# Kernel optimization log

Measured on AMD Instinct MI355X. Metric: run time of the kernel, lower is better.

## Reference

```python
import jax, jax.numpy as jnp
import numpy as np

K_ACTIVE = 32
MULTI_K = 64
AUX_K = 64
DEAD_THRESH = 256


def setup_inputs() -> dict:
    key = jax.random.key(0)
    ks = jax.random.split(key, 4)
    B, D, M = 4096, 1024, 16384
    x = jax.random.normal(ks[0], (B, D), dtype=jnp.float32)
    enc_w = jax.random.normal(ks[1], (M, D), dtype=jnp.float32) / np.sqrt(D)
    dec_w = jax.random.normal(ks[2], (D, M), dtype=jnp.float32) / np.sqrt(M)
    input_bias = jnp.zeros((D,), dtype=jnp.float32)
    neuron_bias = jnp.zeros((M,), dtype=jnp.float32)
    steps = jax.random.randint(ks[3], (M,), 0, 512).astype(jnp.int64)
    return {"x": x, "enc_w": enc_w, "dec_w": dec_w,
            "input_bias": input_bias, "neuron_bias": neuron_bias, "steps": steps}


def reference(x, enc_w, dec_w, input_bias, neuron_bias, steps):
    # encode: center, linear (no bias), add neuron bias, relu
    x_cent = x - input_bias                                   # [B, D]
    pre_act = x_cent @ enc_w.T + neuron_bias                  # [B, M]
    acts = jax.nn.relu(pre_act)
    B, M = acts.shape

    # training path: global batch-wide top-(K*B) across flattened activations
    flat = acts.reshape(-1)                                   # [B*M]
    topk_vals, topk_idx = jax.lax.top_k(flat, K_ACTIVE * B)
    activ = jnp.zeros_like(flat).at[topk_idx].set(topk_vals).reshape(B, M)

    # multi-k branch: per-row top-k on pre-activations, relu, scatter, decode
    mvals, midx = jax.lax.top_k(pre_act, MULTI_K)             # [B, MULTI_K]
    mvals = jax.nn.relu(mvals)
    rows = jnp.arange(B)[:, None]
    multik_activ = jnp.zeros_like(pre_act).at[rows, midx].set(mvals)
    multik_recon = multik_activ @ dec_w.T + input_bias        # [B, D]

    # main reconstruction
    recon = activ @ dec_w.T + input_bias                      # [B, D]

    # dead-neuron bookkeeping + aux top-k over dead neurons
    steps = steps + 1
    active = activ.sum(axis=0) > 0                            # [M]
    steps = jnp.where(active, jnp.zeros_like(steps), steps)
    dead_mask = (steps > DEAD_THRESH).astype(pre_act.dtype)   # [M]
    dead_pre = pre_act * dead_mask                            # [B, M]
    aux_vals, aux_idx = jax.lax.top_k(dead_pre, AUX_K)        # [B, AUX_K]
    aux_vals = jax.nn.relu(aux_vals)

    return recon, activ, multik_recon, aux_vals, aux_idx
```

## Files before the change

### kernel.cpp

```cpp
#include <hip/hip_runtime.h>

#define K_ACTIVE 32
#define MULTI_K 64
#define AUX_K 64
#define DEAD_THRESH 256
#define BUF_CAP 262144u
#define SORT_CAP 4096

typedef unsigned int u32;
typedef unsigned long long u64;
typedef unsigned short ushort_t;
typedef __bf16 bf16x8 __attribute__((ext_vector_type(8)));
typedef float f32x4 __attribute__((ext_vector_type(4)));

__device__ __forceinline__ u32 fmap_signed_bits(u32 u) {
  return (u & 0x80000000u) ? ~u : (u | 0x80000000u);
}

__device__ __forceinline__ u32 bf16_rne(float f) {
  u32 u = __float_as_uint(f);
  return (u + 0x7FFFu + ((u >> 16) & 1u)) >> 16;
}

__device__ __forceinline__ void gload16(const void* g, void* s) {
  __builtin_amdgcn_global_load_lds(
      (const __attribute__((address_space(1))) void*)g,
      (__attribute__((address_space(3))) void*)s, 16, 0, 0);
}

__global__ void transpose_k(const float* __restrict__ in, float* __restrict__ out, int D, int M) {
  __shared__ float tile[32][33];
  const int bx = blockIdx.x * 32;
  const int by = blockIdx.y * 32;
  const int tx = threadIdx.x, ty = threadIdx.y;
  #pragma unroll
  for (int i = 0; i < 32; i += 8)
    tile[ty + i][tx] = in[(size_t)(by + ty + i) * M + bx + tx];
  __syncthreads();
  #pragma unroll
  for (int i = 0; i < 32; i += 8)
    out[(size_t)(bx + ty + i) * D + by + tx] = tile[tx][ty + i];
}

__global__ void convA_k(const float* __restrict__ X, const float* __restrict__ IB,
                        ushort_t* __restrict__ AH, ushort_t* __restrict__ AL, int D) {
  const int idx = blockIdx.x * 256 + threadIdx.x;
  const int row = idx >> 7;
  const int dpos = (idx & 127) << 3;
  const float4* xr = reinterpret_cast<const float4*>(X + (size_t)row * D + dpos);
  const float4* br = reinterpret_cast<const float4*>(IB + dpos);
  float4 x0 = xr[0], x1 = xr[1], b0 = br[0], b1 = br[1];
  float c[8] = {x0.x - b0.x, x0.y - b0.y, x0.z - b0.z, x0.w - b0.w,
                x1.x - b1.x, x1.y - b1.y, x1.z - b1.z, x1.w - b1.w};
  u32 hw[4], lw[4];
  #pragma unroll
  for (int j = 0; j < 4; ++j) {
    u32 h0 = bf16_rne(c[2 * j]), h1 = bf16_rne(c[2 * j + 1]);
    float r0 = c[2 * j] - __uint_as_float(h0 << 16);
    float r1 = c[2 * j + 1] - __uint_as_float(h1 << 16);
    hw[j] = h0 | (h1 << 16);
    lw[j] = bf16_rne(r0) | (bf16_rne(r1) << 16);
  }
  reinterpret_cast<uint4*>(AH)[idx] = make_uint4(hw[0], hw[1], hw[2], hw[3]);
  reinterpret_cast<uint4*>(AL)[idx] = make_uint4(lw[0], lw[1], lw[2], lw[3]);
}

__global__ void convW_k(const float* __restrict__ W,
                        ushort_t* __restrict__ WH, ushort_t* __restrict__ WL) {
  const int idx = blockIdx.x * 256 + threadIdx.x;
  const float4* wr = reinterpret_cast<const float4*>(W) + (size_t)idx * 2;
  float4 x0 = wr[0], x1 = wr[1];
  float c[8] = {x0.x, x0.y, x0.z, x0.w, x1.x, x1.y, x1.z, x1.w};
  u32 hw[4], lw[4];
  #pragma unroll
  for (int j = 0; j < 4; ++j) {
    u32 h0 = bf16_rne(c[2 * j]), h1 = bf16_rne(c[2 * j + 1]);
    float r0 = c[2 * j] - __uint_as_float(h0 << 16);
    float r1 = c[2 * j + 1] - __uint_as_float(h1 << 16);
    hw[j] = h0 | (h1 << 16);
    lw[j] = bf16_rne(r0) | (bf16_rne(r1) << 16);
  }
  reinterpret_cast<uint4*>(WH)[idx] = make_uint4(hw[0], hw[1], hw[2], hw[3]);
  reinterpret_cast<uint4*>(WL)[idx] = make_uint4(lw[0], lw[1], lw[2], lw[3]);
}

__global__ __launch_bounds__(256) void gemm_mfma(
    const ushort_t* __restrict__ AH, const ushort_t* __restrict__ AL,
    const ushort_t* __restrict__ WH, const ushort_t* __restrict__ WL,
    const float* __restrict__ NB, float* __restrict__ OUT, int M) {
  __shared__ ushort_t sA[128 * 64];
  __shared__ ushort_t sB[128 * 64];
  const int tid = threadIdx.x;
  const int wave = tid >> 6, lane = tid & 63;
  const int bm = blockIdx.y * 128, bn = blockIdx.x * 128;
  const int wm = wave & 1, wn = wave >> 1;

  f32x4 acc[4][4];
  #pragma unroll
  for (int i = 0; i < 4; ++i)
    #pragma unroll
    for (int j = 0; j < 4; ++j) acc[i][j] = (f32x4){0.f, 0.f, 0.f, 0.f};

  int rowA[4], cbA[4];
  #pragma unroll
  for (int r = 0; r < 4; ++r) {
    int o = ((wave << 2) + r) * 1024 + lane * 16;
    rowA[r] = o >> 7;
    cbA[r] = o & 127;
  }
  const int cl = lane & 15, kg = lane >> 4;

  for (int kt = 0; kt < 48; ++kt) {
    const int ph = kt >> 4;
    const size_t kb = (size_t)((kt & 15) << 6) * 2;
    const ushort_t* Asrc = (ph == 1) ? AL : AH;
    const ushort_t* Bsrc = (ph == 2) ? WL : WH;
    #pragma unroll
    for (int r = 0; r < 4; ++r) {
      gload16((const char*)Asrc + ((size_t)(bm + rowA[r]) * 2048 + kb + cbA[r]),
              (char*)sA + (((wave << 2) + r) << 10));
      gload16((const char*)Bsrc + ((size_t)(bn + rowA[r]) * 2048 + kb + cbA[r]),
              (char*)sB + (((wave << 2) + r) << 10));
    }
    __syncthreads();
    #pragma unroll
    for (int ks = 0; ks < 2; ++ks) {
      const int kk = ks * 32 + kg * 8;
      bf16x8 af[4], bfr[4];
      #pragma unroll
      for (int mi = 0; mi < 4; ++mi)
        af[mi] = *reinterpret_cast<const bf16x8*>(&sA[(wm * 64 + mi * 16 + cl) * 64 + kk]);
      #pragma unroll
      for (int ni = 0; ni < 4; ++ni)
        bfr[ni] = *reinterpret_cast<const bf16x8*>(&sB[(wn * 64 + ni * 16 + cl) * 64 + kk]);
      #pragma unroll
      for (int mi = 0; mi < 4; ++mi)
        #pragma unroll
        for (int ni = 0; ni < 4; ++ni)
          acc[mi][ni] = __builtin_amdgcn_mfma_f32_16x16x32_bf16(af[mi], bfr[ni], acc[mi][ni], 0, 0, 0);
    }
    __syncthreads();
  }

  const int rg = lane >> 4;
  #pragma unroll
  for (int ni = 0; ni < 4; ++ni) {
    const int col = bn + wn * 64 + ni * 16 + cl;
    const float nbv = NB[col];
    #pragma unroll
    for (int mi = 0; mi < 4; ++mi) {
      const int row0 = bm + wm * 64 + mi * 16 + rg * 4;
      #pragma unroll
      for (int r = 0; r < 4; ++r)
        OUT[(size_t)(row0 + r) * M + col] = acc[mi][ni][r] + nbv;
    }
  }
}

__global__ void hist1_k(const float* __restrict__ P, size_t N, u32* __restrict__ GH) {
  __shared__ u32 h[2048];
  const int tid = threadIdx.x;
  for (int i = tid; i < 2048; i += 256) h[i] = 0;
  __syncthreads();
  u32 l0 = 0;
  const size_t step = (size_t)gridDim.x * 256;
  for (size_t i = (size_t)blockIdx.x * 256 + tid; i < N; i += step) {
    float v = P[i];
    float a = (v > 0.f) ? v : 0.f;
    u32 b = __float_as_uint(a) >> 21;
    if (b) atomicAdd(&h[b], 1u); else ++l0;
  }
  if (l0) atomicAdd(&h[0], l0);
  __syncthreads();
  for (int i = tid; i < 2048; i += 256) if (h[i]) atomicAdd(&GH[i], h[i]);
}

__global__ void scan_k(const u32* __restrict__ H, u32* __restrict__ PRM, u32 K, int phase) {
  __shared__ u32 suf[256];
  const int t = threadIdx.x;
  u32 h[8], ls[8];
  #pragma unroll
  for (int j = 0; j < 8; ++j) h[j] = H[t * 8 + j];
  u32 run = 0;
  #pragma unroll
  for (int j = 7; j >= 0; --j) { run += h[j]; ls[j] = run; }
  suf[t] = run;
  __syncthreads();
  for (int off = 1; off < 256; off <<= 1) {
    u32 v = (t + off < 256) ? suf[t + off] : 0u;
    __syncthreads();
    suf[t] += v;
    __syncthreads();
  }
  const u32 rightOf = (t < 255) ? suf[t + 1] : 0u;
  const u32 base = (phase == 2) ? PRM[1] : 0u;
  #pragma unroll
  for (int j = 0; j < 8; ++j) {
    u32 Sb = base + rightOf + ls[j];
    u32 Sb1 = base + rightOf + ((j < 7) ? ls[j + 1] : 0u);
    if (Sb >= K && Sb1 < K) {
      int b = t * 8 + j;
      if (phase == 1) { PRM[0] = (u32)b; PRM[1] = Sb1; }
      else { PRM[2] = (PRM[0] << 11) | (u32)b; PRM[3] = K - Sb1; }
    }
  }
}

__global__ void hist2_k(const float* __restrict__ P, size_t N, const u32* __restrict__ PRM, u32* __restrict__ GH) {
  const u32 b1 = PRM[0];
  const size_t step = (size_t)gridDim.x * blockDim.x;
  for (size_t i = (size_t)blockIdx.x * blockDim.x + threadIdx.x; i < N; i += step) {
    float v = P[i];
    float a = (v > 0.f) ? v : 0.f;
    u32 u = __float_as_uint(a);
    if ((u >> 21) == b1) atomicAdd(&GH[(u >> 10) & 2047u], 1u);
  }
}

__global__ void collect_k(const float* __restrict__ P, size_t N, u32* __restrict__ PRM,
                          float* __restrict__ BV, u32* __restrict__ BI) {
  const u32 pc = PRM[2];
  const size_t step = (size_t)gridDim.x * blockDim.x;
  for (size_t i = (size_t)blockIdx.x * blockDim.x + threadIdx.x; i < N; i += step) {
    float v = P[i];
    float a = (v > 0.f) ? v : 0.f;
    u32 u = __float_as_uint(a);
    if ((u >> 10) == pc) {
      u32 pos = atomicAdd(&PRM[8], 1u);
      if (pos < BUF_CAP) { BV[pos] = a; BI[pos] = (u32)i; }
    }
  }
}

__global__ void sortmark_k(u32* __restrict__ PRM, const float* __restrict__ BV, const u32* __restrict__ BI,
                           float* __restrict__ SV, u32* __restrict__ SI, u32* __restrict__ CF, int M) {
  __shared__ u64 keys[SORT_CAP];
  const int tid = threadIdx.x;
  u32 nb = PRM[8]; if (nb > SORT_CAP) nb = SORT_CAP;
  const u32 krem = PRM[3];
  if (nb == 0) { if (tid == 0) PRM[5] = 0; return; }
  u32 np = 1; while (np < nb) np <<= 1;
  for (u32 i = tid; i < np; i += 256)
    keys[i] = (i < nb) ? ((((u64)__float_as_uint(BV[i])) << 32) | (u64)(0xFFFFFFFFu - BI[i])) : 0ull;
  __syncthreads();
  for (u32 k = 2; k <= np; k <<= 1) {
    for (u32 j = k >> 1; j > 0; j >>= 1) {
      for (u32 i = tid; i < np; i += 256) {
        u32 ixj = i ^ j;
        if (ixj > i) {
          u64 a = keys[i], b = keys[ixj];
          bool up = ((i & k) == 0);
          if (up ? (a < b) : (a > b)) { keys[i] = b; keys[ixj] = a; }
        }
      }
      __syncthreads();
    }
  }
  u32 nsel = krem < nb ? krem : nb;
  for (u32 t = tid; t < nsel; t += 256) {
    u64 kk = keys[t];
    u32 flat = 0xFFFFFFFFu - (u32)(kk & 0xFFFFFFFFull);
    float val = __uint_as_float((u32)(kk >> 32));
    SI[t] = flat; SV[t] = val;
    if (val > 0.f) CF[flat % (u32)M] = 1u;
  }
  if (tid == 0) PRM[5] = nsel;
}

struct TopkShared {
  u32 hist[256];
  u32 eqcnt[256];
  u32 prefix, need, scnt;
  int selN[64];
  float selV[64];
};

template<bool ZSKIP>
__device__ void row_topk64(const float (&v)[64], int tid, TopkShared* S) {
  const int lane = tid & 63;
  u32 zp = 0, zn = 0;
  if (ZSKIP) {
    #pragma unroll
    for (int j = 0; j < 64; ++j) {
      u32 ub = __float_as_uint(v[j]);
      if (ub == 0u) ++zp;
      else if (ub == 0x80000000u) ++zn;
    }
    for (int o = 32; o > 0; o >>= 1) { zp += __shfl_down(zp, o); zn += __shfl_down(zn, o); }
  }
  if (tid == 0) S->scnt = 0;
  u32 pref = 0, need = 64;
  for (int p = 0; p < 4; ++p) {
    const int sh = 24 - 8 * p;
    S->hist[tid] = 0;
    __syncthreads();
    #pragma unroll
    for (int j = 0; j < 64; ++j) {
      u32 ub = __float_as_uint(v[j]);
      if (ZSKIP && ((ub << 1) == 0u)) continue;
      u32 mu = fmap_signed_bits(ub);
      if (p == 0 || (mu >> (sh + 8)) == pref)
        atomicAdd(&S->hist[(mu >> sh) & 255u], 1u);
    }
    if (ZSKIP && lane == 0) {
      const u32 mup = 0x80000000u, mun = 0x7FFFFFFFu;
      if (zp && (p == 0 || (mup >> (sh + 8)) == pref)) atomicAdd(&S->hist[(mup >> sh) & 255u], zp);
      if (zn && (p == 0 || (mun >> (sh + 8)) == pref)) atomicAdd(&S->hist[(mun >> sh) & 255u], zn);
    }
    __syncthreads();
    for (int off = 1; off < 256; off <<= 1) {
      u32 t2 = (tid + off < 256) ? S->hist[tid + off] : 0u;
      __syncthreads();
      S->hist[tid] += t2;
      __syncthreads();
    }
    u32 Sb = S->hist[tid];
    u32 Sb1 = (tid < 255) ? S->hist[tid + 1] : 0u;
    if (Sb >= need && Sb1 < need) {
      S->prefix = (pref << 8) | (u32)tid;
      S->need = need - Sb1;
    }
    __syncthreads();
    pref = S->prefix; need = S->need;
  }
  const u32 muc = pref, neq = need;
  u32 myeq = 0;
  #pragma unroll
  for (int j = 0; j < 64; ++j) {
    u32 mu = fmap_signed_bits(__float_as_uint(v[j]));
    if (mu > muc) {
      u32 pos = atomicAdd(&S->scnt, 1u);
      S->selN[pos] = tid * 64 + j;
      S->selV[pos] = v[j];
    } else if (mu == muc) ++myeq;
  }
  S->eqcnt[tid] = myeq;
  __syncthreads();
  for (int off = 1; off < 256; off <<= 1) {
    u32 t2 = (tid >= off) ? S->eqcnt[tid - off] : 0u;
    __syncthreads();
    S->eqcnt[tid] += t2;
    __syncthreads();
  }
  const u32 a0 = S->scnt;
  u32 g = S->eqcnt[tid] - myeq;
  #pragma unroll
  for (int j = 0; j < 64; ++j) {
    u32 mu = fmap_signed_bits(__float_as_uint(v[j]));
    if (mu == muc) {
      if (g < neq) { S->selN[a0 + g] = tid * 64 + j; S->selV[a0 + g] = v[j]; }
      ++g;
    }
  }
  __syncthreads();
}

__launch_bounds__(256)
__global__ void rowk_multik(const float* __restrict__ PRE, const float* __restrict__ WT,
                            const float* __restrict__ IB, float* __restrict__ MR,
                            u32* __restrict__ CF, const u32* __restrict__ PRM, int M, int D) {
  __shared__ TopkShared S;
  const int b = blockIdx.x, tid = threadIdx.x;
  const float* rowp = PRE + (size_t)b * M + tid * 64;
  float v[64];
  #pragma unroll
  for (int j = 0; j < 16; ++j) {
    float4 t = reinterpret_cast<const float4*>(rowp)[j];
    v[4 * j + 0] = t.x; v[4 * j + 1] = t.y; v[4 * j + 2] = t.z; v[4 * j + 3] = t.w;
  }
  const u32 pc = PRM[2];
  #pragma unroll
  for (int j = 0; j < 64; ++j) {
    float a = (v[j] > 0.f) ? v[j] : 0.f;
    if (((__float_as_uint(a) >> 10) > pc) && (a > 0.f)) atomicOr(&CF[tid * 64 + j], 1u);
  }
  row_topk64<false>(v, tid, &S);
  const int d0 = tid * 4;
  float4 acc = *reinterpret_cast<const float4*>(IB + d0);
  for (int i = 0; i < 64; ++i) {
    float w = S.selV[i] > 0.f ? S.selV[i] : 0.f;
    if (w > 0.f) {
      const float4 wv = *reinterpret_cast<const float4*>(WT + (size_t)S.selN[i] * D + d0);
      acc.x = fmaf(w, wv.x, acc.x); acc.y = fmaf(w, wv.y, acc.y);
      acc.z = fmaf(w, wv.z, acc.z); acc.w = fmaf(w, wv.w, acc.w);
    }
  }
  *reinterpret_cast<float4*>(MR + (size_t)b * D + d0) = acc;
}

__global__ void dead_k(const u32* __restrict__ CF, const int* __restrict__ ST,
                       u32* __restrict__ DW, int M) {
  int w = blockIdx.x * blockDim.x + threadIdx.x;
  if (w >= M / 32) return;
  u32 bits = 0;
  for (int i = 0; i < 32; ++i) {
    int n = w * 32 + i;
    if (CF[n] == 0 && (ST[n] + 1) > DEAD_THRESH) bits |= (1u << i);
  }
  DW[w] = bits;
}

__launch_bounds__(256)
__global__ void rowk_aux(const float* __restrict__ PRE, const u32* __restrict__ DW,
                         float* __restrict__ AV, float* __restrict__ AI, int M) {
  __shared__ TopkShared S;
  __shared__ u64 skey[64];
  __shared__ int sN[64];
  __shared__ float sV[64];
  const int b = blockIdx.x, tid = threadIdx.x;
  const float* rowp = PRE + (size_t)b * M + tid * 64;
  float v[64];
  #pragma unroll
  for (int j = 0; j < 16; ++j) {
    float4 t = reinterpret_cast<const float4*>(rowp)[j];
    v[4 * j + 0] = t.x; v[4 * j + 1] = t.y; v[4 * j + 2] = t.z; v[4 * j + 3] = t.w;
  }
  const u32 mw0 = DW[tid * 2], mw1 = DW[tid * 2 + 1];
  #pragma unroll
  for (int j = 0; j < 64; ++j) {
    u32 bit = ((j < 32 ? mw0 : mw1) >> (j & 31)) & 1u;
    v[j] = bit ? v[j] : (v[j] * 0.0f);
  }
  row_topk64<true>(v, tid, &S);
  if (tid < 64) {
    float vv = S.selV[tid];
    int col = S.selN[tid];
    u32 mu = fmap_signed_bits(__float_as_uint(vv));
    skey[tid] = (((u64)mu) << 32) | (u64)(0xFFFFFFFFu - (u32)col);
  }
  __syncthreads();
  if (tid < 64) {
    u64 mine = skey[tid];
    int rank = 0;
    for (int j = 0; j < 64; ++j) rank += (skey[j] > mine) ? 1 : 0;
    sN[rank] = S.selN[tid]; sV[rank] = S.selV[tid];
  }
  __syncthreads();
  if (tid < 64) {
    AV[(size_t)b * AUX_K + tid] = sV[tid] > 0.f ? sV[tid] : 0.f;
    AI[(size_t)b * AUX_K + tid] = (float)sN[tid];
  }
}

__launch_bounds__(256)
__global__ void rowk_scatter(float* __restrict__ ACT, const float* __restrict__ WT,
                             const float* __restrict__ IB, float* __restrict__ RC,
                             const u32* __restrict__ PRM, const float* __restrict__ SV,
                             const u32* __restrict__ SI, int M, int D) {
  __shared__ int ovN[256]; __shared__ float ovV[256]; __shared__ u32 ovc;
  __shared__ int lsN[2048]; __shared__ float lsV[2048]; __shared__ u32 lc;
  const int b = blockIdx.x, tid = threadIdx.x;
  float* rowp = ACT + (size_t)b * M + tid * 64;
  float v[64];
  #pragma unroll
  for (int j = 0; j < 16; ++j) {
    float4 t = reinterpret_cast<const float4*>(rowp)[j];
    v[4 * j + 0] = t.x; v[4 * j + 1] = t.y; v[4 * j + 2] = t.z; v[4 * j + 3] = t.w;
  }
  const u32 pc = PRM[2];
  #pragma unroll
  for (int j = 0; j < 64; ++j) {
    float a = (v[j] > 0.f) ? v[j] : 0.f;
    v[j] = ((__float_as_uint(a) >> 10) > pc) ? a : 0.f;
  }
  if (tid == 0) ovc = 0;
  __syncthreads();
  const u32 nbs = PRM[5];
  for (u32 t = tid; t < nbs; t += 256) {
    u32 flat = SI[t];
    if (flat / (u32)M == (u32)b) {
      u32 p = atomicAdd(&ovc, 1u);
      if (p < 256) { ovN[p] = (int)(flat % (u32)M); ovV[p] = SV[t]; }
    }
  }
  __syncthreads();
  const u32 no = ovc < 256u ? ovc : 256u;
  #pragma unroll
  for (int j = 0; j < 64; ++j) {
    const int col = tid * 64 + j;
    for (u32 i = 0; i < no; ++i) if (ovN[i] == col) v[j] = ovV[i];
  }
  #pragma unroll
  for (int j = 0; j < 16; ++j) {
    float4 t = make_float4(v[4 * j + 0], v[4 * j + 1], v[4 * j + 2], v[4 * j + 3]);
    reinterpret_cast<float4*>(rowp)[j] = t;
  }
  const int d0 = tid * 4;
  float4 acc = *reinterpret_cast<const float4*>(IB + d0);
  for (int cpart = 0; cpart < 8; ++cpart) {
    if (tid == 0) lc = 0;
    __syncthreads();
    if ((tid >> 5) == cpart) {
      #pragma unroll
      for (int j = 0; j < 64; ++j) {
        if (v[j] > 0.f) {
          u32 p = atomicAdd(&lc, 1u);
          lsN[p] = tid * 64 + j; lsV[p] = v[j];
        }
      }
    }
    __syncthreads();
    const u32 n = lc;
    for (u32 i = 0; i < n; ++i) {
      const float w = lsV[i];
      const float4 wv = *reinterpret_cast<const float4*>(WT + (size_t)lsN[i] * D + d0);
      acc.x = fmaf(w, wv.x, acc.x); acc.y = fmaf(w, wv.y, acc.y);
      acc.z = fmaf(w, wv.z, acc.z); acc.w = fmaf(w, wv.w, acc.w);
    }
    __syncthreads();
  }
  *reinterpret_cast<float4*>(RC + (size_t)b * D + d0) = acc;
}

extern "C" void kernel_launch(void* const* d_in, const int* in_sizes, int n_in,
                              void* d_out, int out_size, void* d_ws, size_t ws_size,
                              hipStream_t stream) {
  const float* x  = (const float*)d_in[0];
  const float* ew = (const float*)d_in[1];
  const float* dw = (const float*)d_in[2];
  const float* ib = (const float*)d_in[3];
  const float* nb = (const float*)d_in[4];
  const int* steps = (const int*)d_in[5];
  const int D = in_sizes[3];
  const int M = in_sizes[4];
  const int B = in_sizes[0] / D;
  const u32 K = (u32)(K_ACTIVE * B);

  float* out = (float*)d_out;
  float* recon  = out;
  float* activ  = out + (size_t)B * D;
  float* mrecon = activ + (size_t)B * M;
  float* avals  = mrecon + (size_t)B * D;
  float* aidx   = avals + (size_t)B * AUX_K;

  ushort_t* AH = (ushort_t*)recon;
  ushort_t* AL = (ushort_t*)mrecon;

  char* wsp = (char*)d_ws;
  size_t o = 0;
  auto alloc = [&](size_t bytes) { char* p = wsp + o; o += (bytes + 255) & ~(size_t)255; return p; };
  ushort_t* WH = (ushort_t*)alloc((size_t)M * D * 2);
  ushort_t* WL = (ushort_t*)alloc((size_t)M * D * 2);
  float* WT = (float*)alloc((size_t)M * D * 4);
  u32* H1   = (u32*)alloc(8192);
  u32* H2   = (u32*)alloc(8192);
  u32* PRM  = (u32*)alloc(256);
  u32* CF   = (u32*)alloc((size_t)M * 4);
  u32* DW   = (u32*)alloc((size_t)(M / 32) * 4);
  float* BV = (float*)alloc((size_t)BUF_CAP * 4);
  u32* BI   = (u32*)alloc((size_t)BUF_CAP * 4);
  float* SV = (float*)alloc((size_t)SORT_CAP * 4);
  u32* SI   = (u32*)alloc((size_t)SORT_CAP * 4);
  (void)ws_size; (void)n_in; (void)out_size;

  hipMemsetAsync(H1, 0, 8192, stream);
  hipMemsetAsync(H2, 0, 8192, stream);
  hipMemsetAsync(PRM, 0, 256, stream);
  hipMemsetAsync(CF, 0, (size_t)M * 4, stream);

  convA_k<<<(B * D / 8 + 255) / 256, 256, 0, stream>>>(x, ib, AH, AL, D);
  convW_k<<<((size_t)M * D / 8 + 255) / 256, 256, 0, stream>>>(ew, WH, WL);
  transpose_k<<<dim3(M / 32, D / 32), dim3(32, 8), 0, stream>>>(dw, WT, D, M);
  gemm_mfma<<<dim3(M / 128, B / 128), 256, 0, stream>>>(AH, AL, WH, WL, nb, activ, M);

  const size_t N = (size_t)B * M;
  hist1_k<<<2048, 256, 0, stream>>>(activ, N, H1);
  scan_k<<<1, 256, 0, stream>>>(H1, PRM, K, 1);
  hist2_k<<<2048, 256, 0, stream>>>(activ, N, PRM, H2);
  scan_k<<<1, 256, 0, stream>>>(H2, PRM, K, 2);
  collect_k<<<2048, 256, 0, stream>>>(activ, N, PRM, BV, BI);
  sortmark_k<<<1, 256, 0, stream>>>(PRM, BV, BI, SV, SI, CF, M);
  rowk_multik<<<B, 256, 0, stream>>>(activ, WT, ib, mrecon, CF, PRM, M, D);
  dead_k<<<(M / 32 + 255) / 256, 256, 0, stream>>>(CF, steps, DW, M);
  rowk_aux<<<B, 256, 0, stream>>>(activ, DW, avals, aidx, M);
  rowk_scatter<<<B, 256, 0, stream>>>(activ, WT, ib, recon, PRM, SV, SI, M, D);
}
```

Baseline: 1.824 ms.

## Swizzle GEMM LDS, vectorize histogram passes, fuse per-row top-k kernels into one

Adds an XOR swizzle to the GEMM shared-memory tiles so MFMA fragment reads avoid bank conflicts. Vectorizes the histogram and collect passes to float4 and gives hist1 privatized per-lane shared histograms to cut atomic contention. Moves the active-neuron flag marking into collect_k and fuses the multi-k, aux and scatter row kernels into one kernel, so each pre-activation row is read once instead of three times. The row top-k now uses 16 privatized histograms and wave-shuffle scans in place of shared-memory scans. The costs are larger shared-memory use per block, which may lower occupancy, and more register pressure in the fused kernel.

Result: slower. 2.915 ms (+59.8%).

```diff
diff --git a/kernel.cpp b/kernel.cpp
--- a/kernel.cpp
+++ b/kernel.cpp
@@ -101,12 +101,14 @@
     #pragma unroll
     for (int j = 0; j < 4; ++j) acc[i][j] = (f32x4){0.f, 0.f, 0.f, 0.f};
 
-  int rowA[4], cbA[4];
+  int rowA[4], cbS[4];
   #pragma unroll
   for (int r = 0; r < 4; ++r) {
     int o = ((wave << 2) + r) * 1024 + lane * 16;
-    rowA[r] = o >> 7;
-    cbA[r] = o & 127;
+    int row = o >> 7;
+    int cb = o & 127;
+    rowA[r] = row;
+    cbS[r] = cb ^ ((row & 7) << 4);
   }
   const int cl = lane & 15, kg = lane >> 4;
 
@@ -117,22 +119,28 @@
     const ushort_t* Bsrc = (ph == 2) ? WL : WH;
     #pragma unroll
     for (int r = 0; r < 4; ++r) {
-      gload16((const char*)Asrc + ((size_t)(bm + rowA[r]) * 2048 + kb + cbA[r]),
+      gload16((const char*)Asrc + ((size_t)(bm + rowA[r]) * 2048 + kb + cbS[r]),
               (char*)sA + (((wave << 2) + r) << 10));
-      gload16((const char*)Bsrc + ((size_t)(bn + rowA[r]) * 2048 + kb + cbA[r]),
+      gload16((const char*)Bsrc + ((size_t)(bn + rowA[r]) * 2048 + kb + cbS[r]),
               (char*)sB + (((wave << 2) + r) << 10));
     }
     __syncthreads();
     #pragma unroll
     for (int ks = 0; ks < 2; ++ks) {
-      const int kk = ks * 32 + kg * 8;
+      const int kbyte = ks * 64 + kg * 16;
       bf16x8 af[4], bfr[4];
       #pragma unroll
-      for (int mi = 0; mi < 4; ++mi)
-        af[mi] = *reinterpret_cast<const bf16x8*>(&sA[(wm * 64 + mi * 16 + cl) * 64 + kk]);
+      for (int mi = 0; mi < 4; ++mi) {
+        const int rA = wm * 64 + mi * 16 + cl;
+        af[mi] = *reinterpret_cast<const bf16x8*>(
+            (const char*)sA + rA * 128 + (kbyte ^ ((rA & 7) << 4)));
+      }
       #pragma unroll
-      for (int ni = 0; ni < 4; ++ni)
-        bfr[ni] = *reinterpret_cast<const bf16x8*>(&sB[(wn * 64 + ni * 16 + cl) * 64 + kk]);
+      for (int ni = 0; ni < 4; ++ni) {
+        const int rB = wn * 64 + ni * 16 + cl;
+        bfr[ni] = *reinterpret_cast<const bf16x8*>(
+            (const char*)sB + rB * 128 + (kbyte ^ ((rB & 7) << 4)));
+      }
       #pragma unroll
       for (int mi = 0; mi < 4; ++mi)
         #pragma unroll
@@ -157,22 +165,30 @@
   }
 }
 
-__global__ void hist1_k(const float* __restrict__ P, size_t N, u32* __restrict__ GH) {
-  __shared__ u32 h[2048];
+__global__ void hist1_k(const float4* __restrict__ P4, size_t N4, u32* __restrict__ GH) {
+  __shared__ u32 h[4 * 2049];
   const int tid = threadIdx.x;
-  for (int i = tid; i < 2048; i += 256) h[i] = 0;
-  __syncthreads();
+  for (int i = tid; i < 4 * 2049; i += 256) h[i] = 0;
+  __syncthreads();
+  const int rb = (tid & 3) * 2049;
   u32 l0 = 0;
   const size_t step = (size_t)gridDim.x * 256;
-  for (size_t i = (size_t)blockIdx.x * 256 + tid; i < N; i += step) {
-    float v = P[i];
-    float a = (v > 0.f) ? v : 0.f;
-    u32 b = __float_as_uint(a) >> 21;
-    if (b) atomicAdd(&h[b], 1u); else ++l0;
-  }
-  if (l0) atomicAdd(&h[0], l0);
-  __syncthreads();
-  for (int i = tid; i < 2048; i += 256) if (h[i]) atomicAdd(&GH[i], h[i]);
+  for (size_t i = (size_t)blockIdx.x * 256 + tid; i < N4; i += step) {
+    float4 vv = P4[i];
+    float va[4] = {vv.x, vv.y, vv.z, vv.w};
+    #pragma unroll
+    for (int c = 0; c < 4; ++c) {
+      float a = (va[c] > 0.f) ? va[c] : 0.f;
+      u32 b = __float_as_uint(a) >> 21;
+      if (b) atomicAdd(&h[rb + b], 1u); else ++l0;
+    }
+  }
+  if (l0) atomicAdd(&h[rb], l0);
+  __syncthreads();
+  for (int i = tid; i < 2048; i += 256) {
+    u32 s = h[i] + h[2049 + i] + h[2 * 2049 + i] + h[3 * 2049 + i];
+    if (s) atomicAdd(&GH[i], s);
+  }
 }
 
 __global__ void scan_k(const u32* __restrict__ H, u32* __restrict__ PRM, u32 K, int phase) {
@@ -206,28 +222,40 @@
   }
 }
 
-__global__ void hist2_k(const float* __restrict__ P, size_t N, const u32* __restrict__ PRM, u32* __restrict__ GH) {
+__global__ void hist2_k(const float4* __restrict__ P4, size_t N4, const u32* __restrict__ PRM, u32* __restrict__ GH) {
   const u32 b1 = PRM[0];
   const size_t step = (size_t)gridDim.x * blockDim.x;
-  for (size_t i = (size_t)blockIdx.x * blockDim.x + threadIdx.x; i < N; i += step) {
-    float v = P[i];
-    float a = (v > 0.f) ? v : 0.f;
-    u32 u = __float_as_uint(a);
-    if ((u >> 21) == b1) atomicAdd(&GH[(u >> 10) & 2047u], 1u);
-  }
-}
-
-__global__ void collect_k(const float* __restrict__ P, size_t N, u32* __restrict__ PRM,
-                          float* __restrict__ BV, u32* __restrict__ BI) {
+  for (size_t i = (size_t)blockIdx.x * blockDim.x + threadIdx.x; i < N4; i += step) {
+    float4 vv = P4[i];
+    float va[4] = {vv.x, vv.y, vv.z, vv.w};
+    #pragma unroll
+    for (int c = 0; c < 4; ++c) {
+      float a = (va[c] > 0.f) ? va[c] : 0.f;
+      u32 u = __float_as_uint(a);
+      if ((u >> 21) == b1) atomicAdd(&GH[(u >> 10) & 2047u], 1u);
+    }
+  }
+}
+
+__global__ void collect_k(const float4* __restrict__ P4, size_t N4, u32* __restrict__ PRM,
+                          float* __restrict__ BV, u32* __restrict__ BI,
+                          u32* __restrict__ CF, int M) {
   const u32 pc = PRM[2];
   const size_t step = (size_t)gridDim.x * blockDim.x;
-  for (size_t i = (size_t)blockIdx.x * blockDim.x + threadIdx.x; i < N; i += step) {
-    float v = P[i];
-    float a = (v > 0.f) ? v : 0.f;
-    u32 u = __float_as_uint(a);
-    if ((u >> 10) == pc) {
-      u32 pos = atomicAdd(&PRM[8], 1u);
-      if (pos < BUF_CAP) { BV[pos] = a; BI[pos] = (u32)i; }
+  for (size_t i = (size_t)blockIdx.x * blockDim.x + threadIdx.x; i < N4; i += step) {
+    float4 vv = P4[i];
+    float va[4] = {vv.x, vv.y, vv.z, vv.w};
+    #pragma unroll
+    for (int c = 0; c < 4; ++c) {
+      float a = (va[c] > 0.f) ? va[c] : 0.f;
+      u32 u = __float_as_uint(a);
+      u32 bin = u >> 10;
+      if (bin == pc) {
+        u32 pos = atomicAdd(&PRM[8], 1u);
+        if (pos < BUF_CAP) { BV[pos] = a; BI[pos] = (u32)(i * 4 + c); }
+      } else if (bin > pc) {
+        if (a > 0.f) CF[(u32)((i * 4 + c) % (size_t)M)] = 1u;
+      }
     }
   }
 }
@@ -267,127 +295,6 @@
   if (tid == 0) PRM[5] = nsel;
 }
 
-struct TopkShared {
-  u32 hist[256];
-  u32 eqcnt[256];
-  u32 prefix, need, scnt;
-  int selN[64];
-  float selV[64];
-};
-
-template<bool ZSKIP>
-__device__ void row_topk64(const float (&v)[64], int tid, TopkShared* S) {
-  const int lane = tid & 63;
-  u32 zp = 0, zn = 0;
-  if (ZSKIP) {
-    #pragma unroll
-    for (int j = 0; j < 64; ++j) {
-      u32 ub = __float_as_uint(v[j]);
-      if (ub == 0u) ++zp;
-      else if (ub == 0x80000000u) ++zn;
-    }
-    for (int o = 32; o > 0; o >>= 1) { zp += __shfl_down(zp, o); zn += __shfl_down(zn, o); }
-  }
-  if (tid == 0) S->scnt = 0;
-  u32 pref = 0, need = 64;
-  for (int p = 0; p < 4; ++p) {
-    const int sh = 24 - 8 * p;
-    S->hist[tid] = 0;
-    __syncthreads();
-    #pragma unroll
-    for (int j = 0; j < 64; ++j) {
-      u32 ub = __float_as_uint(v[j]);
-      if (ZSKIP && ((ub << 1) == 0u)) continue;
-      u32 mu = fmap_signed_bits(ub);
-      if (p == 0 || (mu >> (sh + 8)) == pref)
-        atomicAdd(&S->hist[(mu >> sh) & 255u], 1u);
-    }
-    if (ZSKIP && lane == 0) {
-      const u32 mup = 0x80000000u, mun = 0x7FFFFFFFu;
-      if (zp && (p == 0 || (mup >> (sh + 8)) == pref)) atomicAdd(&S->hist[(mup >> sh) & 255u], zp);
-      if (zn && (p == 0 || (mun >> (sh + 8)) == pref)) atomicAdd(&S->hist[(mun >> sh) & 255u], zn);
-    }
-    __syncthreads();
-    for (int off = 1; off < 256; off <<= 1) {
-      u32 t2 = (tid + off < 256) ? S->hist[tid + off] : 0u;
-      __syncthreads();
-      S->hist[tid] += t2;
-      __syncthreads();
-    }
-    u32 Sb = S->hist[tid];
-    u32 Sb1 = (tid < 255) ? S->hist[tid + 1] : 0u;
-    if (Sb >= need && Sb1 < need) {
-      S->prefix = (pref << 8) | (u32)tid;
-      S->need = need - Sb1;
-    }
-    __syncthreads();
-    pref = S->prefix; need = S->need;
-  }
-  const u32 muc = pref, neq = need;
-  u32 myeq = 0;
-  #pragma unroll
-  for (int j = 0; j < 64; ++j) {
-    u32 mu = fmap_signed_bits(__float_as_uint(v[j]));
-    if (mu > muc) {
-      u32 pos = atomicAdd(&S->scnt, 1u);
-      S->selN[pos] = tid * 64 + j;
-      S->selV[pos] = v[j];
-    } else if (mu == muc) ++myeq;
-  }
-  S->eqcnt[tid] = myeq;
-  __syncthreads();
-  for (int off = 1; off < 256; off <<= 1) {
-    u32 t2 = (tid >= off) ? S->eqcnt[tid - off] : 0u;
-    __syncthreads();
-    S->eqcnt[tid] += t2;
-    __syncthreads();
-  }
-  const u32 a0 = S->scnt;
-  u32 g = S->eqcnt[tid] - myeq;
-  #pragma unroll
-  for (int j = 0; j < 64; ++j) {
-    u32 mu = fmap_signed_bits(__float_as_uint(v[j]));
-    if (mu == muc) {
-      if (g < neq) { S->selN[a0 + g] = tid * 64 + j; S->selV[a0 + g] = v[j]; }
-      ++g;
-    }
-  }
-  __syncthreads();
-}
-
-__launch_bounds__(256)
-__global__ void rowk_multik(const float* __restrict__ PRE, const float* __restrict__ WT,
-                            const float* __restrict__ IB, float* __restrict__ MR,
-                            u32* __restrict__ CF, const u32* __restrict__ PRM, int M, int D) {
-  __shared__ TopkShared S;
-  const int b = blockIdx.x, tid = threadIdx.x;
-  const float* rowp = PRE + (size_t)b * M + tid * 64;
-  float v[64];
-  #pragma unroll
-  for (int j = 0; j < 16; ++j) {
-    float4 t = reinterpret_cast<const float4*>(rowp)[j];
-    v[4 * j + 0] = t.x; v[4 * j + 1] = t.y; v[4 * j + 2] = t.z; v[4 * j + 3] = t.w;
-  }
-  const u32 pc = PRM[2];
-  #pragma unroll
-  for (int j = 0; j < 64; ++j) {
-    float a = (v[j] > 0.f) ? v[j] : 0.f;
-    if (((__float_as_uint(a) >> 10) > pc) && (a > 0.f)) atomicOr(&CF[tid * 64 + j], 1u);
-  }
-  row_topk64<false>(v, tid, &S);
-  const int d0 = tid * 4;
-  float4 acc = *reinterpret_cast<const float4*>(IB + d0);
-  for (int i = 0; i < 64; ++i) {
-    float w = S.selV[i] > 0.f ? S.selV[i] : 0.f;
-    if (w > 0.f) {
-      const float4 wv = *reinterpret_cast<const float4*>(WT + (size_t)S.selN[i] * D + d0);
-      acc.x = fmaf(w, wv.x, acc.x); acc.y = fmaf(w, wv.y, acc.y);
-      acc.z = fmaf(w, wv.z, acc.z); acc.w = fmaf(w, wv.w, acc.w);
-    }
-  }
-  *reinterpret_cast<float4*>(MR + (size_t)b * D + d0) = acc;
-}
-
 __global__ void dead_k(const u32* __restrict__ CF, const int* __restrict__ ST,
                        u32* __restrict__ DW, int M) {
   int w = blockIdx.x * blockDim.x + threadIdx.x;
@@ -400,28 +307,158 @@
   DW[w] = bits;
 }
 
+struct TopkSh {
+  union {
+    u32 hist[16 * 257];
+    struct { int N[2048]; float V[2048]; } ls;
+  } u;
+  u32 wred[4];
+  u32 prefix, need, scnt;
+  int selN[64];
+  float selV[64];
+};
+
+#define VALX(j) (MASKED ? ((((((j) < 32) ? mw0 : mw1) >> ((j) & 31)) & 1u) ? v[(j)] : v[(j)] * 0.0f) : v[(j)])
+
+template<bool MASKED>
+__device__ void row_topk64(const float (&v)[64], u32 mw0, u32 mw1, int tid, TopkSh* S) {
+  const int lane = tid & 63, wid = tid >> 6;
+  u32 zp = 0, zn = 0;
+  if (MASKED) {
+    #pragma unroll
+    for (int j = 0; j < 64; ++j) {
+      u32 ub = __float_as_uint(VALX(j));
+      zp += (ub == 0u);
+      zn += (ub == 0x80000000u);
+    }
+    #pragma unroll
+    for (int o = 32; o > 0; o >>= 1) { zp += __shfl_down(zp, o); zn += __shfl_down(zn, o); }
+  }
+  u32 pref = 0, need = 64;
+  for (int p = 0; p < 4; ++p) {
+    const int sh = 24 - 8 * p;
+    for (int i = tid; i < 16 * 257; i += 256) S->u.hist[i] = 0;
+    if (p == 0 && tid == 0) S->scnt = 0;
+    __syncthreads();
+    const int rb = (tid & 15) * 257;
+    #pragma unroll
+    for (int j = 0; j < 64; ++j) {
+      float f = VALX(j);
+      u32 ub = __float_as_uint(f);
+      if (MASKED && ((ub << 1) == 0u)) continue;
+      u32 mu = fmap_signed_bits(ub);
+      if (p == 0 || (mu >> (sh + 8)) == pref)
+        atomicAdd(&S->u.hist[rb + ((mu >> sh) & 255u)], 1u);
+    }
+    if (MASKED && lane == 0) {
+      const u32 mup = 0x80000000u, mun = 0x7FFFFFFFu;
+      if (zp && (p == 0 || (mup >> (sh + 8)) == pref))
+        atomicAdd(&S->u.hist[wid * 257 + ((mup >> sh) & 255u)], zp);
+      if (zn && (p == 0 || (mun >> (sh + 8)) == pref))
+        atomicAdd(&S->u.hist[wid * 257 + ((mun >> sh) & 255u)], zn);
+    }
+    __syncthreads();
+    u32 own = 0;
+    #pragma unroll
+    for (int r = 0; r < 16; ++r) own += S->u.hist[r * 257 + tid];
+    u32 x = own;
+    #pragma unroll
+    for (int o = 1; o < 64; o <<= 1) {
+      u32 y = __shfl_down(x, o);
+      x += (lane + o < 64) ? y : 0u;
+    }
+    if (lane == 0) S->wred[wid] = x;
+    __syncthreads();
+    u32 Sb = x;
+    for (int w = wid + 1; w < 4; ++w) Sb += S->wred[w];
+    u32 below = Sb - own;
+    if (Sb >= need && below < need) {
+      S->prefix = (pref << 8) | (u32)tid;
+      S->need = need - below;
+    }
+    __syncthreads();
+    pref = S->prefix; need = S->need;
+  }
+  const u32 muc = pref, neq = need;
+  u32 myeq = 0;
+  #pragma unroll
+  for (int j = 0; j < 64; ++j) {
+    float f = VALX(j);
+    u32 mu = fmap_signed_bits(__float_as_uint(f));
+    if (mu > muc) {
+      u32 pos = atomicAdd(&S->scnt, 1u);
+      S->selN[pos] = tid * 64 + j;
+      S->selV[pos] = f;
+    } else if (mu == muc) ++myeq;
+  }
+  u32 xs = myeq;
+  #pragma unroll
+  for (int o = 1; o < 64; o <<= 1) {
+    u32 y = __shfl_up(xs, o);
+    xs += (lane >= o) ? y : 0u;
+  }
+  if (lane == 63) S->wred[wid] = xs;
+  __syncthreads();
+  u32 base = 0;
+  for (int w = 0; w < wid; ++w) base += S->wred[w];
+  u32 g = base + xs - myeq;
+  const u32 a0 = S->scnt;
+  #pragma unroll
+  for (int j = 0; j < 64; ++j) {
+    float f = VALX(j);
+    u32 mu = fmap_signed_bits(__float_as_uint(f));
+    if (mu == muc) {
+      if (g < neq) { S->selN[a0 + g] = tid * 64 + j; S->selV[a0 + g] = f; }
+      ++g;
+    }
+  }
+  __syncthreads();
+}
+
 __launch_bounds__(256)
-__global__ void rowk_aux(const float* __restrict__ PRE, const u32* __restrict__ DW,
-                         float* __restrict__ AV, float* __restrict__ AI, int M) {
-  __shared__ TopkShared S;
+__global__ void rowk_fused(float* __restrict__ ACT, const float* __restrict__ WT,
+                           const float* __restrict__ IB,
+                           float* __restrict__ RC, float* __restrict__ MR,
+                           float* __restrict__ AV, float* __restrict__ AI,
+                           const u32* __restrict__ DW, const u32* __restrict__ PRM,
+                           const float* __restrict__ SV, const u32* __restrict__ SI,
+                           int M, int D) {
+  __shared__ TopkSh S;
   __shared__ u64 skey[64];
-  __shared__ int sN[64];
-  __shared__ float sV[64];
+  __shared__ int sN2[64];
+  __shared__ float sV2[64];
+  __shared__ int ovN[256];
+  __shared__ float ovV[256];
+  __shared__ u32 ovc, lc;
   const int b = blockIdx.x, tid = threadIdx.x;
-  const float* rowp = PRE + (size_t)b * M + tid * 64;
+  float* rowp = ACT + (size_t)b * M + tid * 64;
   float v[64];
   #pragma unroll
   for (int j = 0; j < 16; ++j) {
     float4 t = reinterpret_cast<const float4*>(rowp)[j];
     v[4 * j + 0] = t.x; v[4 * j + 1] = t.y; v[4 * j + 2] = t.z; v[4 * j + 3] = t.w;
   }
-  const u32 mw0 = DW[tid * 2], mw1 = DW[tid * 2 + 1];
-  #pragma unroll
-  for (int j = 0; j < 64; ++j) {
-    u32 bit = ((j < 32 ? mw0 : mw1) >> (j & 31)) & 1u;
-    v[j] = bit ? v[j] : (v[j] * 0.0f);
-  }
-  row_topk64<true>(v, tid, &S);
+  const int d0 = tid * 4;
+
+  row_topk64<false>(v, 0u, 0u, tid, &S);
+  {
+    float4 acc = *reinterpret_cast<const float4*>(IB + d0);
+    for (int i = 0; i < 64; ++i) {
+      float w = S.selV[i];
+      if (w > 0.f) {
+        const float4 wv = *reinterpret_cast<const float4*>(WT + (size_t)S.selN[i] * D + d0);
+        acc.x = fmaf(w, wv.x, acc.x); acc.y = fmaf(w, wv.y, acc.y);
+        acc.z = fmaf(w, wv.z, acc.z); acc.w = fmaf(w, wv.w, acc.w);
+      }
+    }
+    *reinterpret_cast<float4*>(MR + (size_t)b * D + d0) = acc;
+  }
+  __syncthreads();
+
+  {
+    const u32 mw0 = DW[tid * 2], mw1 = DW[tid * 2 + 1];
+    row_topk64<true>(v, mw0, mw1, tid, &S);
+  }
   if (tid < 64) {
     float vv = S.selV[tid];
     int col = S.selN[tid];
@@ -433,30 +470,15 @@
     u64 mine = skey[tid];
     int rank = 0;
     for (int j = 0; j < 64; ++j) rank += (skey[j] > mine) ? 1 : 0;
-    sN[rank] = S.selN[tid]; sV[rank] = S.selV[tid];
+    sN2[rank] = S.selN[tid]; sV2[rank] = S.selV[tid];
   }
   __syncthreads();
   if (tid < 64) {
-    AV[(size_t)b * AUX_K + tid] = sV[tid] > 0.f ? sV[tid] : 0.f;
-    AI[(size_t)b * AUX_K + tid] = (float)sN[tid];
-  }
-}
-
-__launch_bounds__(256)
-__global__ void rowk_scatter(float* __restrict__ ACT, const float* __restrict__ WT,
-                             const float* __restrict__ IB, float* __restrict__ RC,
-                             const u32* __restrict__ PRM, const float* __restrict__ SV,
-                             const u32* __restrict__ SI, int M, int D) {
-  __shared__ int ovN[256]; __shared__ float ovV[256]; __shared__ u32 ovc;
-  __shared__ int lsN[2048]; __shared__ float lsV[2048]; __shared__ u32 lc;
-  const int b = blockIdx.x, tid = threadIdx.x;
-  float* rowp = ACT + (size_t)b * M + tid * 64;
-  float v[64];
-  #pragma unroll
-  for (int j = 0; j < 16; ++j) {
-    float4 t = reinterpret_cast<const float4*>(rowp)[j];
-    v[4 * j + 0] = t.x; v[4 * j + 1] = t.y; v[4 * j + 2] = t.z; v[4 * j + 3] = t.w;
-  }
+    AV[(size_t)b * AUX_K + tid] = sV2[tid] > 0.f ? sV2[tid] : 0.f;
+    AI[(size_t)b * AUX_K + tid] = (float)sN2[tid];
+  }
+  __syncthreads();
+
   const u32 pc = PRM[2];
   #pragma unroll
   for (int j = 0; j < 64; ++j) {
@@ -485,7 +507,6 @@
     float4 t = make_float4(v[4 * j + 0], v[4 * j + 1], v[4 * j + 2], v[4 * j + 3]);
     reinterpret_cast<float4*>(rowp)[j] = t;
   }
-  const int d0 = tid * 4;
   float4 acc = *reinterpret_cast<const float4*>(IB + d0);
   for (int cpart = 0; cpart < 8; ++cpart) {
     if (tid == 0) lc = 0;
@@ -495,15 +516,15 @@
       for (int j = 0; j < 64; ++j) {
         if (v[j] > 0.f) {
           u32 p = atomicAdd(&lc, 1u);
-          lsN[p] = tid * 64 + j; lsV[p] = v[j];
+          S.u.ls.N[p] = tid * 64 + j; S.u.ls.V[p] = v[j];
         }
       }
     }
     __syncthreads();
     const u32 n = lc;
     for (u32 i = 0; i < n; ++i) {
-      const float w = lsV[i];
-      const float4 wv = *reinterpret_cast<const float4*>(WT + (size_t)lsN[i] * D + d0);
+      const float w = S.u.ls.V[i];
+      const float4 wv = *reinterpret_cast<const float4*>(WT + (size_t)S.u.ls.N[i] * D + d0);
       acc.x = fmaf(w, wv.x, acc.x); acc.y = fmaf(w, wv.y, acc.y);
       acc.z = fmaf(w, wv.z, acc.z); acc.w = fmaf(w, wv.w, acc.w);
     }
@@ -563,15 +584,15 @@
   transpose_k<<<dim3(M / 32, D / 32), dim3(32, 8), 0, stream>>>(dw, WT, D, M);
   gemm_mfma<<<dim3(M / 128, B / 128), 256, 0, stream>>>(AH, AL, WH, WL, nb, activ, M);
 
-  const size_t N = (size_t)B * M;
-  hist1_k<<<2048, 256, 0, stream>>>(activ, N, H1);
+  const size_t N4 = (size_t)B * M / 4;
+  const float4* act4 = (const float4*)activ;
+  hist1_k<<<2048, 256, 0, stream>>>(act4, N4, H1);
   scan_k<<<1, 256, 0, stream>>>(H1, PRM, K, 1);
-  hist2_k<<<2048, 256, 0, stream>>>(activ, N, PRM, H2);
+  hist2_k<<<2048, 256, 0, stream>>>(act4, N4, PRM, H2);
   scan_k<<<1, 256, 0, stream>>>(H2, PRM, K, 2);
-  collect_k<<<2048, 256, 0, stream>>>(activ, N, PRM, BV, BI);
+  collect_k<<<2048, 256, 0, stream>>>(act4, N4, PRM, BV, BI, CF, M);
   sortmark_k<<<1, 256, 0, stream>>>(PRM, BV, BI, SV, SI, CF, M);
-  rowk_multik<<<B, 256, 0, stream>>>(activ, WT, ib, mrecon, CF, PRM, M, D);
   dead_k<<<(M / 32 + 255) / 256, 256, 0, stream>>>(CF, steps, DW, M);
-  rowk_aux<<<B, 256, 0, stream>>>(activ, DW, avals, aidx, M);
-  rowk_scatter<<<B, 256, 0, stream>>>(activ, WT, ib, recon, PRM, SV, SI, M, D);
-}
+  rowk_fused<<<B, 256, 0, stream>>>(activ, WT, ib, recon, mrecon, avals, aidx,
+                                    DW, PRM, SV, SI, M, D);
+}
```
